# Performance work log

Measured on AMD Instinct MI355X. Metric: run time of the kernel, lower is better.

Reference implementation:

```python
import jax, jax.numpy as jnp
import numpy as np

D = 8388608  # vector_dim
N = 1024     # phase table size
M = 1024     # magnitude table size


def setup_inputs() -> dict:
    key = jax.random.key(0)
    k1, k2, k3, k4 = jax.random.split(key, 4)
    ctx_phase_idx = jax.random.randint(k1, (D,), 0, N, dtype=jnp.int64)
    ctx_mag_idx = jax.random.randint(k2, (D,), 0, M, dtype=jnp.int64)
    self_phase_idx = jax.random.randint(k3, (D,), 0, N, dtype=jnp.int64)
    self_mag_idx = jax.random.randint(k4, (D,), 0, M, dtype=jnp.int64)
    # Lookup tables (the ExtendedLookupTableModule's precomputed tables):
    # phase table = cos(2*pi*i/N), its grad = -sin(2*pi*i/N) * (2*pi/N)
    # magnitude table = exp(linspace), its grad = same exp * slope
    phase_grid = 2.0 * jnp.pi * jnp.arange(N, dtype=jnp.float32) / N
    mag_grid = jnp.linspace(-1.0, 1.0, M, dtype=jnp.float32)
    cos_table = jnp.cos(phase_grid)
    cos_grad_table = -jnp.sin(phase_grid) * (2.0 * jnp.pi / N)
    exp_table = jnp.exp(mag_grid)
    exp_grad_table = exp_table * (2.0 / (M - 1))
    return {
        "ctx_phase_idx": ctx_phase_idx,
        "ctx_mag_idx": ctx_mag_idx,
        "self_phase_idx": self_phase_idx,
        "self_mag_idx": self_mag_idx,
        "cos_table": cos_table,
        "exp_table": exp_table,
        "cos_grad_table": cos_grad_table,
        "exp_grad_table": exp_grad_table,
    }


def reference(ctx_phase_idx, ctx_mag_idx, self_phase_idx, self_mag_idx,
              cos_table, exp_table, cos_grad_table, exp_grad_table):
    # mod-indexed sums
    phase_out = (ctx_phase_idx + self_phase_idx) % N  # [D] int
    mag_out = (ctx_mag_idx + self_mag_idx) % M        # [D] int
    # four table gathers
    cos_vals = cos_table[phase_out]       # [D]
    exp_vals = exp_table[mag_out]         # [D]
    dcos = cos_grad_table[phase_out]      # [D]
    dexp = exp_grad_table[mag_out]        # [D]
    # elementwise multiplies + reduction
    signal = cos_vals * exp_vals          # [D]
    grad_phase = dcos * exp_vals          # [D]
    grad_mag = cos_vals * dexp            # [D]
    strength = signal.sum()
    return (phase_out, mag_out, signal, strength, grad_phase, grad_mag)
```

## Files before the change

### kernel.cpp

```cpp
#include <hip/hip_runtime.h>

constexpr int D_TOTAL = 8388608;
constexpr int TBL = 1024;
constexpr int IDX_MASK = 1023;
constexpr int BLOCK = 256;
constexpr int VEC = 8;
constexpr int ELEMS_PER_BLOCK = BLOCK * VEC;
constexpr int NBLOCKS = D_TOTAL / ELEMS_PER_BLOCK;

typedef float f32x4 __attribute__((ext_vector_type(4)));
typedef float f32x8 __attribute__((ext_vector_type(8)));
typedef int   i32x8 __attribute__((ext_vector_type(8)));
typedef f32x4 f32x4u __attribute__((aligned(4)));

__global__ __launch_bounds__(BLOCK) void phasecell_main(
    const int* __restrict__ ctx_p, const int* __restrict__ ctx_m,
    const int* __restrict__ self_p, const int* __restrict__ self_m,
    const float* __restrict__ cos_t, const float* __restrict__ exp_t,
    const float* __restrict__ dcos_t, const float* __restrict__ dexp_t,
    float* __restrict__ out, float* __restrict__ block_sums) {
  __shared__ float2 s_phase[TBL];
  __shared__ float2 s_mag[TBL];
  for (int i = threadIdx.x; i < TBL; i += BLOCK) {
    s_phase[i] = make_float2(cos_t[i], dcos_t[i]);
    s_mag[i]   = make_float2(exp_t[i], dexp_t[i]);
  }
  __syncthreads();

  const int base = (blockIdx.x * BLOCK + threadIdx.x) * VEC;

  const i32x8 cp = *reinterpret_cast<const i32x8*>(ctx_p + base);
  const i32x8 cm = *reinterpret_cast<const i32x8*>(ctx_m + base);
  const i32x8 sp = *reinterpret_cast<const i32x8*>(self_p + base);
  const i32x8 sm = *reinterpret_cast<const i32x8*>(self_m + base);

  int p[VEC], m[VEC];
#pragma unroll
  for (int j = 0; j < VEC; ++j) {
    p[j] = (cp[j] + sp[j]) & IDX_MASK;
    m[j] = (cm[j] + sm[j]) & IDX_MASK;
  }

  f32x8 po, mo, sig;
  f32x4 gph0, gph1, gmg0, gmg1;
  float local = 0.f;
#pragma unroll
  for (int j = 0; j < VEC; ++j) {
    const float2 ph = s_phase[p[j]];
    const float2 mg = s_mag[m[j]];
    const float s = ph.x * mg.x;
    sig[j] = s;
    const float gp = ph.y * mg.x;
    const float gm = ph.x * mg.y;
    if (j < 4) { gph0[j] = gp; gmg0[j] = gm; }
    else       { gph1[j - 4] = gp; gmg1[j - 4] = gm; }
    po[j] = (float)p[j];
    mo[j] = (float)m[j];
    local += s;
  }

  *reinterpret_cast<f32x8*>(out + base)                = po;
  *reinterpret_cast<f32x8*>(out + D_TOTAL + base)      = mo;
  *reinterpret_cast<f32x8*>(out + 2 * D_TOTAL + base)  = sig;

  float* gp_base = out + 3 * D_TOTAL + 1 + base;
  float* gm_base = out + 4 * D_TOTAL + 1 + base;
  *reinterpret_cast<f32x4u*>(gp_base)     = gph0;
  *reinterpret_cast<f32x4u*>(gp_base + 4) = gph1;
  *reinterpret_cast<f32x4u*>(gm_base)     = gmg0;
  *reinterpret_cast<f32x4u*>(gm_base + 4) = gmg1;

#pragma unroll
  for (int off = 32; off > 0; off >>= 1) local += __shfl_down(local, off, 64);
  __shared__ float wsum[BLOCK / 64];
  const int wave = threadIdx.x >> 6;
  const int lane = threadIdx.x & 63;
  if (lane == 0) wsum[wave] = local;
  __syncthreads();
  if (threadIdx.x == 0) {
    float t = 0.f;
#pragma unroll
    for (int w = 0; w < BLOCK / 64; ++w) t += wsum[w];
    block_sums[blockIdx.x] = t;
  }
}

__global__ __launch_bounds__(BLOCK) void phasecell_reduce(
    const float* __restrict__ partials, float* __restrict__ strength_out) {
  float s = 0.f;
  for (int i = threadIdx.x; i < NBLOCKS; i += BLOCK) s += partials[i];
#pragma unroll
  for (int off = 32; off > 0; off >>= 1) s += __shfl_down(s, off, 64);
  __shared__ float wsum[BLOCK / 64];
  const int wave = threadIdx.x >> 6;
  const int lane = threadIdx.x & 63;
  if (lane == 0) wsum[wave] = s;
  __syncthreads();
  if (threadIdx.x == 0) {
    float t = 0.f;
#pragma unroll
    for (int w = 0; w < BLOCK / 64; ++w) t += wsum[w];
    strength_out[0] = t;
  }
}

extern "C" void kernel_launch(void* const* d_in, const int* in_sizes, int n_in,
                              void* d_out, int out_size, void* d_ws, size_t ws_size,
                              hipStream_t stream) {
  const int* ctx_p  = (const int*)d_in[0];
  const int* ctx_m  = (const int*)d_in[1];
  const int* self_p = (const int*)d_in[2];
  const int* self_m = (const int*)d_in[3];
  const float* cos_t  = (const float*)d_in[4];
  const float* exp_t  = (const float*)d_in[5];
  const float* dcos_t = (const float*)d_in[6];
  const float* dexp_t = (const float*)d_in[7];
  float* out = (float*)d_out;
  float* block_sums = (float*)d_ws;

  phasecell_main<<<NBLOCKS, BLOCK, 0, stream>>>(
      ctx_p, ctx_m, self_p, self_m, cos_t, exp_t, dcos_t, dexp_t, out, block_sums);
  phasecell_reduce<<<1, BLOCK, 0, stream>>>(block_sums, out + 3 * (size_t)D_TOTAL);
}
```

Baseline: 290.7 us.

## Realign gradient output stores by shifting values across lanes

```diff
diff --git a/kernel.cpp b/kernel.cpp
--- a/kernel.cpp
+++ b/kernel.cpp
@@ -11,7 +11,7 @@
 typedef float f32x4 __attribute__((ext_vector_type(4)));
 typedef float f32x8 __attribute__((ext_vector_type(8)));
 typedef int   i32x8 __attribute__((ext_vector_type(8)));
-typedef f32x4 f32x4u __attribute__((aligned(4)));
+typedef float f32x2 __attribute__((ext_vector_type(2)));
 
 __global__ __launch_bounds__(BLOCK) void phasecell_main(
     const int* __restrict__ ctx_p, const int* __restrict__ ctx_m,
@@ -19,6 +19,15 @@
     const float* __restrict__ cos_t, const float* __restrict__ exp_t,
     const float* __restrict__ dcos_t, const float* __restrict__ dexp_t,
     float* __restrict__ out, float* __restrict__ block_sums) {
+  const int base = (blockIdx.x * BLOCK + threadIdx.x) * VEC;
+
+  int cpp = 0, spp = 0, cpm = 0, spm = 0;
+  const bool need_prev = (threadIdx.x == 0) && (blockIdx.x != 0);
+  if (need_prev) {
+    cpp = ctx_p[base - 1];  spp = self_p[base - 1];
+    cpm = ctx_m[base - 1];  spm = self_m[base - 1];
+  }
+
   __shared__ float2 s_phase[TBL];
   __shared__ float2 s_mag[TBL];
   for (int i = threadIdx.x; i < TBL; i += BLOCK) {
@@ -26,8 +35,6 @@
     s_mag[i]   = make_float2(exp_t[i], dexp_t[i]);
   }
   __syncthreads();
-
-  const int base = (blockIdx.x * BLOCK + threadIdx.x) * VEC;
 
   const i32x8 cp = *reinterpret_cast<const i32x8*>(ctx_p + base);
   const i32x8 cm = *reinterpret_cast<const i32x8*>(ctx_m + base);
@@ -41,40 +48,73 @@
     m[j] = (cm[j] + sm[j]) & IDX_MASK;
   }
 
-  f32x8 po, mo, sig;
-  f32x4 gph0, gph1, gmg0, gmg1;
+  f32x8 po, mo, sg;
+  float gpv[VEC], gmv[VEC];
   float local = 0.f;
 #pragma unroll
   for (int j = 0; j < VEC; ++j) {
     const float2 ph = s_phase[p[j]];
     const float2 mg = s_mag[m[j]];
     const float s = ph.x * mg.x;
-    sig[j] = s;
-    const float gp = ph.y * mg.x;
-    const float gm = ph.x * mg.y;
-    if (j < 4) { gph0[j] = gp; gmg0[j] = gm; }
-    else       { gph1[j - 4] = gp; gmg1[j - 4] = gm; }
+    sg[j] = s;
+    gpv[j] = ph.y * mg.x;
+    gmv[j] = ph.x * mg.y;
     po[j] = (float)p[j];
     mo[j] = (float)m[j];
     local += s;
   }
 
-  *reinterpret_cast<f32x8*>(out + base)                = po;
-  *reinterpret_cast<f32x8*>(out + D_TOTAL + base)      = mo;
-  *reinterpret_cast<f32x8*>(out + 2 * D_TOTAL + base)  = sig;
+  *reinterpret_cast<f32x8*>(out + base)               = po;
+  *reinterpret_cast<f32x8*>(out + D_TOTAL + base)     = mo;
+  *reinterpret_cast<f32x8*>(out + 2 * D_TOTAL + base) = sg;
 
-  float* gp_base = out + 3 * D_TOTAL + 1 + base;
-  float* gm_base = out + 4 * D_TOTAL + 1 + base;
-  *reinterpret_cast<f32x4u*>(gp_base)     = gph0;
-  *reinterpret_cast<f32x4u*>(gp_base + 4) = gph1;
-  *reinterpret_cast<f32x4u*>(gm_base)     = gmg0;
-  *reinterpret_cast<f32x4u*>(gm_base + 4) = gmg1;
+  float pgp = __shfl_up(gpv[VEC - 1], 1);
+  float pgm = __shfl_up(gmv[VEC - 1], 1);
+  __shared__ float wlast_gp[BLOCK / 64], wlast_gm[BLOCK / 64];
+  const int wave = threadIdx.x >> 6;
+  const int lane = threadIdx.x & 63;
+  if (lane == 63) { wlast_gp[wave] = gpv[VEC - 1]; wlast_gm[wave] = gmv[VEC - 1]; }
+  __syncthreads();
+  if (lane == 0) {
+    if (wave > 0) {
+      pgp = wlast_gp[wave - 1];
+      pgm = wlast_gm[wave - 1];
+    } else if (blockIdx.x != 0) {
+      const int pp = (cpp + spp) & IDX_MASK;
+      const int pm = (cpm + spm) & IDX_MASK;
+      const float2 ph = s_phase[pp];
+      const float2 mg = s_mag[pm];
+      pgp = ph.y * mg.x;
+      pgm = ph.x * mg.y;
+    }
+  }
+
+  f32x8 gpo, gmo;
+  gpo[0] = pgp;  gmo[0] = pgm;
+#pragma unroll
+  for (int j = 1; j < VEC; ++j) { gpo[j] = gpv[j - 1]; gmo[j] = gmv[j - 1]; }
+
+  if (base != 0) {
+    *reinterpret_cast<f32x8*>(out + 3 * D_TOTAL + base) = gpo;
+    *reinterpret_cast<f32x8*>(out + 4 * D_TOTAL + base) = gmo;
+  } else {
+    float* g0 = out + 3 * D_TOTAL;
+    float* g1 = out + 4 * D_TOTAL;
+    g0[1] = gpo[1];
+    g1[1] = gmo[1];
+    *reinterpret_cast<f32x2*>(g0 + 2) = f32x2{gpo[2], gpo[3]};
+    *reinterpret_cast<f32x2*>(g1 + 2) = f32x2{gmo[2], gmo[3]};
+    *reinterpret_cast<f32x4*>(g0 + 4) = f32x4{gpo[4], gpo[5], gpo[6], gpo[7]};
+    *reinterpret_cast<f32x4*>(g1 + 4) = f32x4{gmo[4], gmo[5], gmo[6], gmo[7]};
+  }
+  if (base == D_TOTAL - VEC) {
+    out[4 * D_TOTAL] = gpv[VEC - 1];
+    out[5 * D_TOTAL] = gmv[VEC - 1];
+  }
 
 #pragma unroll
   for (int off = 32; off > 0; off >>= 1) local += __shfl_down(local, off, 64);
   __shared__ float wsum[BLOCK / 64];
-  const int wave = threadIdx.x >> 6;
-  const int lane = threadIdx.x & 63;
   if (lane == 0) wsum[wave] = local;
   __syncthreads();
   if (threadIdx.x == 0) {
```

Measured after the change: 288.7 us. Within noise of the previous version (-0.7%).
